# Kernel optimization log

Measured on AMD Instinct MI355X. Metric: run time of the kernel, lower is better.

## Reference

```python
import jax, jax.numpy as jnp
import numpy as np

N_NODES = 50000
N_EDGES = 600000
IN_DIM = 128
HID = 256
OUT = 3


def setup_inputs() -> dict:
    key = jax.random.key(0)
    ks = jax.random.split(key, 10)
    x = jax.random.normal(ks[0], (N_NODES, IN_DIM), dtype=jnp.float32)
    edge_index = jax.random.randint(ks[1], (2, N_EDGES), 0, N_NODES, dtype=jnp.int64)
    s = lambda k, shp: jax.random.normal(k, shp, dtype=jnp.float32) * (1.0 / np.sqrt(shp[0]))
    return {
        "x": x,
        "edge_index": edge_index,
        # SAGEConv1: lin_l (applied to aggregated neighbors, with bias), lin_r (root, no bias)
        "W1l": s(ks[2], (IN_DIM, HID)), "b1": jnp.zeros((HID,), jnp.float32), "W1r": s(ks[3], (IN_DIM, HID)),
        # SAGEConv2
        "W2l": s(ks[4], (HID, HID)), "b2": jnp.zeros((HID,), jnp.float32), "W2r": s(ks[5], (HID, HID)),
        # classification head
        "Wh": s(ks[6], (HID, OUT)), "bh": jnp.zeros((OUT,), jnp.float32),
    }


def _sage_conv(x, edge_index, Wl, b, Wr):
    """PyG SAGEConv with mean aggregation: out = lin_l(mean_{j->i} x_j) + lin_r(x_i)."""
    src, dst = edge_index[0], edge_index[1]
    n = x.shape[0]
    # gather source features and scatter-mean onto targets
    msg_sum = jax.ops.segment_sum(x[src], dst, num_segments=n)          # [N, d]
    deg = jax.ops.segment_sum(jnp.ones((src.shape[0],), x.dtype), dst, num_segments=n)
    mean = msg_sum / jnp.maximum(deg, 1.0)[:, None]                      # isolated nodes -> 0
    return mean @ Wl + b + x @ Wr


def reference(x, edge_index, W1l, b1, W1r, W2l, b2, W2r, Wh, bh):
    h = jax.nn.relu(_sage_conv(x, edge_index, W1l, b1, W1r))
    # dropout(p=0.2) is identity in eval mode
    h = jax.nn.relu(_sage_conv(h, edge_index, W2l, b2, W2r))
    return h @ Wh + bh
```

## Files before the change

### kernel.cpp

```cpp
#include <hip/hip_runtime.h>
#include <hip/hip_bf16.h>

#define N_NODES 50000
#define N_EDGES 600000
#define IN_DIM 128
#define HID 256
#define OUT_DIM 3

#define M_PAD 50048

#define SCAN_B 256
#define SCAN_NB ((N_NODES + SCAN_B - 1) / SCAN_B)

typedef __bf16 bf16x8 __attribute__((ext_vector_type(8)));
typedef float f32x4 __attribute__((ext_vector_type(4)));

static __device__ __forceinline__ unsigned short f2b(float f) {
    union { float f; unsigned u; } u; u.f = f;
    unsigned r = u.u + 0x7fffu + ((u.u >> 16) & 1u);
    return (unsigned short)(r >> 16);
}
static __device__ __forceinline__ float b2f(unsigned short b) {
    union { unsigned u; float f; } u; u.u = ((unsigned)b) << 16;
    return u.f;
}

static __device__ __forceinline__ size_t swz(int r, int k, int K) {
    return (((size_t)((r >> 4) * (K >> 5) + (k >> 5))) << 9)
         + ((((k >> 3) & 3) * 16 + (r & 15)) << 3) + (k & 7);
}


__global__ void count_deg_kernel(const int* __restrict__ dst, int* __restrict__ counts) {
    int e = blockIdx.x * blockDim.x + threadIdx.x;
    if (e < N_EDGES) atomicAdd(&counts[dst[e]], 1);
}

__global__ __launch_bounds__(256) void block_sum_kernel(const int* __restrict__ counts,
                                                        int* __restrict__ partial) {
    int node = blockIdx.x * SCAN_B + threadIdx.x;
    int v = (node < N_NODES) ? counts[node] : 0;
#pragma unroll
    for (int off = 32; off > 0; off >>= 1) v += __shfl_down(v, off);
    __shared__ int ws[4];
    if ((threadIdx.x & 63) == 0) ws[threadIdx.x >> 6] = v;
    __syncthreads();
    if (threadIdx.x == 0) partial[blockIdx.x] = ws[0] + ws[1] + ws[2] + ws[3];
}

__global__ __launch_bounds__(256) void scan_partial_kernel(int* __restrict__ partial) {
    __shared__ int s[SCAN_B];
    int t = threadIdx.x;
    int v = (t < SCAN_NB) ? partial[t] : 0;
    s[t] = v;
    __syncthreads();
    for (int off = 1; off < SCAN_B; off <<= 1) {
        int u = (t >= off) ? s[t - off] : 0;
        __syncthreads();
        s[t] += u;
        __syncthreads();
    }
    if (t < SCAN_NB) partial[t] = s[t] - v;
}

__global__ __launch_bounds__(256) void write_rowptr_kernel(const int* __restrict__ counts,
                                                           const int* __restrict__ partial,
                                                           int* __restrict__ row_ptr) {
    __shared__ int s[SCAN_B];
    int t = threadIdx.x;
    int node = blockIdx.x * SCAN_B + t;
    int v = (node < N_NODES) ? counts[node] : 0;
    s[t] = v;
    __syncthreads();
    for (int off = 1; off < SCAN_B; off <<= 1) {
        int u = (t >= off) ? s[t - off] : 0;
        __syncthreads();
        s[t] += u;
        __syncthreads();
    }
    if (node < N_NODES) row_ptr[node] = partial[blockIdx.x] + s[t] - v;
    if (node == 0) row_ptr[N_NODES] = N_EDGES;
}

__global__ void fill_csr_kernel(const int* __restrict__ src, const int* __restrict__ dst,
                                const int* __restrict__ row_ptr, int* __restrict__ cursor,
                                int* __restrict__ csr_src) {
    int e = blockIdx.x * blockDim.x + threadIdx.x;
    if (e < N_EDGES) {
        int d = dst[e];
        int pos = atomicAdd(&cursor[d], 1);
        csr_src[row_ptr[d] + pos] = src[e];
    }
}


__global__ void cast_f2b_kernel(const float* __restrict__ in,
                                unsigned short* __restrict__ out_row,
                                unsigned short* __restrict__ out_swz) {
    int i = blockIdx.x * blockDim.x + threadIdx.x;
    if (i * 4 < N_NODES * IN_DIM) {
        float4 v = ((const float4*)in)[i];
        ushort4 o;
        o.x = f2b(v.x); o.y = f2b(v.y); o.z = f2b(v.z); o.w = f2b(v.w);
        ((ushort4*)out_row)[i] = o;
        int m = i >> 5;
        int kb = (i & 31) * 4;
        *(ushort4*)(out_swz + swz(m, kb, IN_DIM)) = o;
    }
}

__global__ void tcast4_kernel(const float* __restrict__ W1l, const float* __restrict__ W1r,
                              const float* __restrict__ W2l, const float* __restrict__ W2r,
                              unsigned short* __restrict__ W1lt, unsigned short* __restrict__ W1rt,
                              unsigned short* __restrict__ W2lt, unsigned short* __restrict__ W2rt) {
    int i = blockIdx.x * blockDim.x + threadIdx.x;
    const float* in; unsigned short* out; int K, base;
    if (i < 32768)        { in = W1l; out = W1lt; K = IN_DIM; base = 0; }
    else if (i < 65536)   { in = W1r; out = W1rt; K = IN_DIM; base = 32768; }
    else if (i < 131072)  { in = W2l; out = W2lt; K = HID;    base = 65536; }
    else if (i < 196608)  { in = W2r; out = W2rt; K = HID;    base = 131072; }
    else return;
    int j = i - base;
    int k = j >> 8;
    int n = j & 255;
    out[swz(n, k, K)] = f2b(in[j]);
}

__global__ void init_out_kernel(const float* __restrict__ bh, float* __restrict__ out) {
    int i = blockIdx.x * blockDim.x + threadIdx.x;
    if (i < N_NODES * 3) out[i] = bh[i % 3];
}


static __device__ __forceinline__ void addv(float* acc, uint4 v) {
    acc[0] += b2f((unsigned short)(v.x & 0xffff));
    acc[1] += b2f((unsigned short)(v.x >> 16));
    acc[2] += b2f((unsigned short)(v.y & 0xffff));
    acc[3] += b2f((unsigned short)(v.y >> 16));
    acc[4] += b2f((unsigned short)(v.z & 0xffff));
    acc[5] += b2f((unsigned short)(v.z >> 16));
    acc[6] += b2f((unsigned short)(v.w & 0xffff));
    acc[7] += b2f((unsigned short)(v.w >> 16));
}

static __device__ __forceinline__ uint4 pack8(const float* a) {
    uint4 pk;
    pk.x = (unsigned)f2b(a[0]) | ((unsigned)f2b(a[1]) << 16);
    pk.y = (unsigned)f2b(a[2]) | ((unsigned)f2b(a[3]) << 16);
    pk.z = (unsigned)f2b(a[4]) | ((unsigned)f2b(a[5]) << 16);
    pk.w = (unsigned)f2b(a[6]) | ((unsigned)f2b(a[7]) << 16);
    return pk;
}

__global__ __launch_bounds__(256) void agg_mean256_kernel(const unsigned short* __restrict__ feat,
                                                          const int* __restrict__ row_ptr,
                                                          const int* __restrict__ csr_src,
                                                          unsigned short* __restrict__ out_swz) {
    int node = blockIdx.x * 4 + (threadIdx.x >> 6);
    if (node >= N_NODES) return;
    int lane = threadIdx.x & 63;
    int half = lane >> 5, lh = lane & 31;
    const uint4* f4 = (const uint4*)feat;
    float acc[8];
#pragma unroll
    for (int j = 0; j < 8; j++) acc[j] = 0.f;
    int beg = row_ptr[node], end = row_ptr[node + 1];
    int i = beg;
    for (; i + 4 <= end; i += 4) {
        int sA = csr_src[i + half];
        int sB = csr_src[i + 2 + half];
        uint4 vA = f4[(size_t)sA * 32 + lh];
        uint4 vB = f4[(size_t)sB * 32 + lh];
        addv(acc, vA);
        addv(acc, vB);
    }
    if (i + 2 <= end) {
        int s = csr_src[i + half];
        addv(acc, f4[(size_t)s * 32 + lh]);
        i += 2;
    }
    if (i < end && half == 0) {
        int s = csr_src[i];
        addv(acc, f4[(size_t)s * 32 + lh]);
    }
    float inv = (end > beg) ? 1.0f / (float)(end - beg) : 0.0f;
#pragma unroll
    for (int j = 0; j < 8; j++) {
        acc[j] += __shfl_xor(acc[j], 32);
        acc[j] *= inv;
    }
    if (half == 0) *(uint4*)(out_swz + swz(node, lh * 8, HID)) = pack8(acc);
}

__global__ __launch_bounds__(256) void agg_mean128_kernel(const unsigned short* __restrict__ feat,
                                                          const int* __restrict__ row_ptr,
                                                          const int* __restrict__ csr_src,
                                                          unsigned short* __restrict__ out_swz) {
    int node = blockIdx.x * 4 + (threadIdx.x >> 6);
    if (node >= N_NODES) return;
    int lane = threadIdx.x & 63;
    int q = lane >> 4, lq = lane & 15;
    const uint4* f4 = (const uint4*)feat;
    float acc[8];
#pragma unroll
    for (int j = 0; j < 8; j++) acc[j] = 0.f;
    int beg = row_ptr[node], end = row_ptr[node + 1];
    int i = beg;
    for (; i + 8 <= end; i += 8) {
        int sA = csr_src[i + q];
        int sB = csr_src[i + 4 + q];
        uint4 vA = f4[(size_t)sA * 16 + lq];
        uint4 vB = f4[(size_t)sB * 16 + lq];
        addv(acc, vA);
        addv(acc, vB);
    }
    if (i + 4 <= end) {
        int s = csr_src[i + q];
        addv(acc, f4[(size_t)s * 16 + lq]);
        i += 4;
    }
    int rem = end - i;
    if (q < rem) {
        int s = csr_src[i + q];
        addv(acc, f4[(size_t)s * 16 + lq]);
    }
    float inv = (end > beg) ? 1.0f / (float)(end - beg) : 0.0f;
#pragma unroll
    for (int j = 0; j < 8; j++) {
        acc[j] += __shfl_xor(acc[j], 32);
        acc[j] += __shfl_xor(acc[j], 16);
        acc[j] *= inv;
    }
    if (q == 0) *(uint4*)(out_swz + swz(node, lq * 8, IN_DIM)) = pack8(acc);
}


template <int KP>
static __device__ __forceinline__ void gemm_swz_core64(
    const unsigned short* __restrict__ A0, const unsigned short* __restrict__ B0,
    const unsigned short* __restrict__ A1, const unsigned short* __restrict__ B1,
    int tmw, int tn0, int l, f32x4 (&acc)[2][4]) {
    constexpr int KT = KP / 32;
    constexpr int TT = 2 * KT;
    bf16x8 a[2][2], b[2][4];

#define LDTILE(t_, s_)                                                                     \
    {                                                                                      \
        const unsigned short* A_ = ((t_) < KT) ? A0 : A1;                                  \
        const unsigned short* B_ = ((t_) < KT) ? B0 : B1;                                  \
        const int tk_ = ((t_) < KT) ? (t_) : (t_) - KT;                                    \
        a[s_][0] = *(const bf16x8*)(A_ + ((((size_t)tmw) * KT + tk_) << 9) + l * 8);       \
        a[s_][1] = *(const bf16x8*)(A_ + ((((size_t)(tmw + 1)) * KT + tk_) << 9) + l * 8); \
        _Pragma("unroll")                                                                  \
        for (int nt = 0; nt < 4; nt++)                                                     \
            b[s_][nt] = *(const bf16x8*)(B_ + ((((size_t)(tn0 + nt)) * KT + tk_) << 9) + l * 8); \
    }

    LDTILE(0, 0)
#pragma unroll
    for (int t = 0; t < TT; t++) {
        const int cur = t & 1;
        if (t + 1 < TT) LDTILE(t + 1, cur ^ 1)
#pragma unroll
        for (int mt = 0; mt < 2; mt++)
#pragma unroll
            for (int nt = 0; nt < 4; nt++)
                acc[mt][nt] = __builtin_amdgcn_mfma_f32_16x16x32_bf16(a[cur][mt], b[cur][nt],
                                                                      acc[mt][nt], 0, 0, 0);
    }
#undef LDTILE
}

template <int KP>
__global__ __launch_bounds__(256) void gemm_swz_kernel(
    const unsigned short* __restrict__ A0, const unsigned short* __restrict__ B0,
    const unsigned short* __restrict__ A1, const unsigned short* __restrict__ B1,
    const float* __restrict__ bias, unsigned short* __restrict__ out_row,
    unsigned short* __restrict__ out_swz, int M) {
    const int t = threadIdx.x;
    const int w = t >> 6, l = t & 63;
    const int quad = l >> 4, lr = l & 15;
    const int n0 = blockIdx.x * 64, m0 = blockIdx.y * 128;
    const int tmw = (m0 >> 4) + w * 2, tn0 = n0 >> 4;

    f32x4 acc[2][4];
    const f32x4 zero = {0.f, 0.f, 0.f, 0.f};
#pragma unroll
    for (int mt = 0; mt < 2; mt++)
#pragma unroll
        for (int nt = 0; nt < 4; nt++) acc[mt][nt] = zero;

    float bias_r[4];
#pragma unroll
    for (int nt = 0; nt < 4; nt++) bias_r[nt] = bias[n0 + nt * 16 + lr];

    gemm_swz_core64<KP>(A0, B0, A1, B1, tmw, tn0, l, acc);

#pragma unroll
    for (int mt = 0; mt < 2; mt++)
#pragma unroll
        for (int r = 0; r < 4; r++) {
            int gm = m0 + w * 32 + mt * 16 + quad * 4 + r;
            if (gm >= M) continue;
            unsigned short* orow = out_row + (size_t)gm * HID;
#pragma unroll
            for (int nt = 0; nt < 4; nt++) {
                int gn = n0 + nt * 16 + lr;
                unsigned short h = f2b(fmaxf(acc[mt][nt][r] + bias_r[nt], 0.f));
                orow[gn] = h;
                out_swz[swz(gm, gn, HID)] = h;
            }
        }
}

template <int KP>
__global__ __launch_bounds__(256) void gemm_swz_head_kernel(
    const unsigned short* __restrict__ A0, const unsigned short* __restrict__ B0,
    const unsigned short* __restrict__ A1, const unsigned short* __restrict__ B1,
    const float* __restrict__ bias, const float* __restrict__ Wh,
    float* __restrict__ out, int M) {
    const int t = threadIdx.x;
    const int w = t >> 6, l = t & 63;
    const int quad = l >> 4, lr = l & 15;
    const int n0 = blockIdx.x * 64, m0 = blockIdx.y * 128;
    const int tmw = (m0 >> 4) + w * 2, tn0 = n0 >> 4;

    f32x4 acc[2][4];
    const f32x4 zero = {0.f, 0.f, 0.f, 0.f};
#pragma unroll
    for (int mt = 0; mt < 2; mt++)
#pragma unroll
        for (int nt = 0; nt < 4; nt++) acc[mt][nt] = zero;

    float bias_r[4];
    float wh_r[4][3];
#pragma unroll
    for (int nt = 0; nt < 4; nt++) {
        int gn = n0 + nt * 16 + lr;
        bias_r[nt] = bias[gn];
        wh_r[nt][0] = Wh[gn * 3 + 0];
        wh_r[nt][1] = Wh[gn * 3 + 1];
        wh_r[nt][2] = Wh[gn * 3 + 2];
    }

    gemm_swz_core64<KP>(A0, B0, A1, B1, tmw, tn0, l, acc);

#pragma unroll
    for (int mt = 0; mt < 2; mt++)
#pragma unroll
        for (int r = 0; r < 4; r++) {
            int gm = m0 + w * 32 + mt * 16 + quad * 4 + r;
            float p0 = 0.f, p1 = 0.f, p2 = 0.f;
#pragma unroll
            for (int nt = 0; nt < 4; nt++) {
                float v = fmaxf(acc[mt][nt][r] + bias_r[nt], 0.f);
                p0 += v * wh_r[nt][0];
                p1 += v * wh_r[nt][1];
                p2 += v * wh_r[nt][2];
            }
#pragma unroll
            for (int off = 1; off < 16; off <<= 1) {
                p0 += __shfl_xor(p0, off);
                p1 += __shfl_xor(p1, off);
                p2 += __shfl_xor(p2, off);
            }
            if (lr == 0 && gm < M) {
                atomicAdd(&out[(size_t)gm * 3 + 0], p0);
                atomicAdd(&out[(size_t)gm * 3 + 1], p1);
                atomicAdd(&out[(size_t)gm * 3 + 2], p2);
            }
        }
}


extern "C" void kernel_launch(void* const* d_in, const int* in_sizes, int n_in,
                              void* d_out, int out_size, void* d_ws, size_t ws_size,
                              hipStream_t stream) {
    const float* x   = (const float*)d_in[0];
    const int*   ei  = (const int*)d_in[1];
    const int*   src = ei;
    const int*   dst = ei + N_EDGES;
    const float* W1l = (const float*)d_in[2];
    const float* b1  = (const float*)d_in[3];
    const float* W1r = (const float*)d_in[4];
    const float* W2l = (const float*)d_in[5];
    const float* b2  = (const float*)d_in[6];
    const float* W2r = (const float*)d_in[7];
    const float* Wh  = (const float*)d_in[8];
    const float* bh  = (const float*)d_in[9];
    float* out = (float*)d_out;

    char* ws = (char*)d_ws;
    size_t off = 0;
    auto alloc = [&](size_t bytes) -> void* {
        void* p = ws + off;
        off = (off + bytes + 255) & ~(size_t)255;
        return p;
    };
    int* counts   = (int*)alloc((size_t)N_NODES * 4);
    int* row_ptr  = (int*)alloc((size_t)(N_NODES + 1) * 4);
    int* cursor   = (int*)alloc((size_t)N_NODES * 4);
    int* partial  = (int*)alloc((size_t)SCAN_NB * 4);
    int* csr_src  = (int*)alloc((size_t)N_EDGES * 4);
    unsigned short* xb_row  = (unsigned short*)alloc((size_t)M_PAD * IN_DIM * 2);
    unsigned short* xb_swz  = (unsigned short*)alloc((size_t)M_PAD * IN_DIM * 2);
    unsigned short* agg1    = (unsigned short*)alloc((size_t)M_PAD * IN_DIM * 2);
    unsigned short* h1_row  = (unsigned short*)alloc((size_t)M_PAD * HID * 2);
    unsigned short* h1_swz  = (unsigned short*)alloc((size_t)M_PAD * HID * 2);
    unsigned short* agg2    = (unsigned short*)alloc((size_t)M_PAD * HID * 2);
    unsigned short* W1lt = (unsigned short*)alloc((size_t)IN_DIM * HID * 2);
    unsigned short* W1rt = (unsigned short*)alloc((size_t)IN_DIM * HID * 2);
    unsigned short* W2lt = (unsigned short*)alloc((size_t)HID * HID * 2);
    unsigned short* W2rt = (unsigned short*)alloc((size_t)HID * HID * 2);

    hipMemsetAsync(counts, 0, (size_t)N_NODES * 4, stream);
    hipMemsetAsync(cursor, 0, (size_t)N_NODES * 4, stream);

    const int eblocks = (N_EDGES + 255) / 256;
    count_deg_kernel<<<eblocks, 256, 0, stream>>>(dst, counts);
    block_sum_kernel<<<SCAN_NB, SCAN_B, 0, stream>>>(counts, partial);
    scan_partial_kernel<<<1, SCAN_B, 0, stream>>>(partial);
    write_rowptr_kernel<<<SCAN_NB, SCAN_B, 0, stream>>>(counts, partial, row_ptr);
    fill_csr_kernel<<<eblocks, 256, 0, stream>>>(src, dst, row_ptr, cursor, csr_src);

    {
        int n = N_NODES * IN_DIM;
        cast_f2b_kernel<<<(n / 4 + 255) / 256, 256, 0, stream>>>(x, xb_row, xb_swz);
        tcast4_kernel<<<(196608 + 255) / 256, 256, 0, stream>>>(W1l, W1r, W2l, W2r,
                                                                W1lt, W1rt, W2lt, W2rt);
        init_out_kernel<<<(N_NODES * 3 + 255) / 256, 256, 0, stream>>>(bh, out);
    }

    const int nblocks4 = (N_NODES + 3) / 4;
    dim3 gg(4, M_PAD / 128);

    agg_mean128_kernel<<<nblocks4, 256, 0, stream>>>(xb_row, row_ptr, csr_src, agg1);
    gemm_swz_kernel<IN_DIM><<<gg, 256, 0, stream>>>(agg1, W1lt, xb_swz, W1rt, b1,
                                                    h1_row, h1_swz, N_NODES);

    agg_mean256_kernel<<<nblocks4, 256, 0, stream>>>(h1_row, row_ptr, csr_src, agg2);
    gemm_swz_head_kernel<HID><<<gg, 256, 0, stream>>>(agg2, W2lt, h1_swz, W2rt, b2, Wh,
                                                      out, N_NODES);
}
```

Baseline: 311.9 us.

## Deepen GEMM register prefetch to 4 stages and remap blocks into grouped panels

The GEMM core now keeps four register buffers and prefetches three k-tiles ahead instead of double-buffering, so global load latency is better hidden behind MFMA work. The 2D grid becomes a 1D grid that groups 8 row panels with all 4 column tiles, so blocks that share A panels run close together and hit in L2. Launch bounds request 3 blocks per CU. The extra buffers raise register pressure, which may cut occupancy or cause spills.

Result: faster. 302.1 us (-3.2%).

```diff
diff --git a/kernel.cpp b/kernel.cpp
--- a/kernel.cpp
+++ b/kernel.cpp
@@ -8,6 +8,7 @@
 #define OUT_DIM 3
 
 #define M_PAD 50048
+#define N_PANELS 391
 
 #define SCAN_B 256
 #define SCAN_NB ((N_NODES + SCAN_B - 1) / SCAN_B)
@@ -236,31 +237,31 @@
 
 
 template <int KP>
-static __device__ __forceinline__ void gemm_swz_core64(
+static __device__ __forceinline__ void gemm_swz_core_pd4(
     const unsigned short* __restrict__ A0, const unsigned short* __restrict__ B0,
     const unsigned short* __restrict__ A1, const unsigned short* __restrict__ B1,
     int tmw, int tn0, int l, f32x4 (&acc)[2][4]) {
     constexpr int KT = KP / 32;
     constexpr int TT = 2 * KT;
-    bf16x8 a[2][2], b[2][4];
-
-#define LDTILE(t_, s_)                                                                     \
-    {                                                                                      \
-        const unsigned short* A_ = ((t_) < KT) ? A0 : A1;                                  \
-        const unsigned short* B_ = ((t_) < KT) ? B0 : B1;                                  \
-        const int tk_ = ((t_) < KT) ? (t_) : (t_) - KT;                                    \
-        a[s_][0] = *(const bf16x8*)(A_ + ((((size_t)tmw) * KT + tk_) << 9) + l * 8);       \
-        a[s_][1] = *(const bf16x8*)(A_ + ((((size_t)(tmw + 1)) * KT + tk_) << 9) + l * 8); \
-        _Pragma("unroll")                                                                  \
-        for (int nt = 0; nt < 4; nt++)                                                     \
-            b[s_][nt] = *(const bf16x8*)(B_ + ((((size_t)(tn0 + nt)) * KT + tk_) << 9) + l * 8); \
-    }
-
-    LDTILE(0, 0)
+    bf16x8 a[4][2], b[4][4];
+
+    auto ldtile = [&](int t_, int s_) {
+        const unsigned short* A_ = (t_ < KT) ? A0 : A1;
+        const unsigned short* B_ = (t_ < KT) ? B0 : B1;
+        const int tk_ = (t_ < KT) ? t_ : t_ - KT;
+        a[s_][0] = *(const bf16x8*)(A_ + ((((size_t)tmw) * KT + tk_) << 9) + l * 8);
+        a[s_][1] = *(const bf16x8*)(A_ + ((((size_t)(tmw + 1)) * KT + tk_) << 9) + l * 8);
+#pragma unroll
+        for (int nt = 0; nt < 4; nt++)
+            b[s_][nt] = *(const bf16x8*)(B_ + ((((size_t)(tn0 + nt)) * KT + tk_) << 9) + l * 8);
+    };
+
+#pragma unroll
+    for (int p = 0; p < 3; p++) ldtile(p, p);
 #pragma unroll
     for (int t = 0; t < TT; t++) {
-        const int cur = t & 1;
-        if (t + 1 < TT) LDTILE(t + 1, cur ^ 1)
+        const int cur = t & 3;
+        if (t + 3 < TT) ldtile(t + 3, (t + 3) & 3);
 #pragma unroll
         for (int mt = 0; mt < 2; mt++)
 #pragma unroll
@@ -268,19 +269,21 @@
                 acc[mt][nt] = __builtin_amdgcn_mfma_f32_16x16x32_bf16(a[cur][mt], b[cur][nt],
                                                                       acc[mt][nt], 0, 0, 0);
     }
-#undef LDTILE
 }
 
 template <int KP>
-__global__ __launch_bounds__(256) void gemm_swz_kernel(
+__global__ __launch_bounds__(256, 3) void gemm_swz_kernel(
     const unsigned short* __restrict__ A0, const unsigned short* __restrict__ B0,
     const unsigned short* __restrict__ A1, const unsigned short* __restrict__ B1,
     const float* __restrict__ bias, unsigned short* __restrict__ out_row,
     unsigned short* __restrict__ out_swz, int M) {
+    const int bid = blockIdx.x;
+    const int panel = (bid >> 5) * 8 + (bid & 7);
+    if (panel >= N_PANELS) return;
     const int t = threadIdx.x;
     const int w = t >> 6, l = t & 63;
     const int quad = l >> 4, lr = l & 15;
-    const int n0 = blockIdx.x * 64, m0 = blockIdx.y * 128;
+    const int m0 = panel * 128, n0 = ((bid >> 3) & 3) * 64;
     const int tmw = (m0 >> 4) + w * 2, tn0 = n0 >> 4;
 
     f32x4 acc[2][4];
@@ -294,7 +297,7 @@
 #pragma unroll
     for (int nt = 0; nt < 4; nt++) bias_r[nt] = bias[n0 + nt * 16 + lr];
 
-    gemm_swz_core64<KP>(A0, B0, A1, B1, tmw, tn0, l, acc);
+    gemm_swz_core_pd4<KP>(A0, B0, A1, B1, tmw, tn0, l, acc);
 
 #pragma unroll
     for (int mt = 0; mt < 2; mt++)
@@ -314,15 +317,18 @@
 }
 
 template <int KP>
-__global__ __launch_bounds__(256) void gemm_swz_head_kernel(
+__global__ __launch_bounds__(256, 3) void gemm_swz_head_kernel(
     const unsigned short* __restrict__ A0, const unsigned short* __restrict__ B0,
     const unsigned short* __restrict__ A1, const unsigned short* __restrict__ B1,
     const float* __restrict__ bias, const float* __restrict__ Wh,
     float* __restrict__ out, int M) {
+    const int bid = blockIdx.x;
+    const int panel = (bid >> 5) * 8 + (bid & 7);
+    if (panel >= N_PANELS) return;
     const int t = threadIdx.x;
     const int w = t >> 6, l = t & 63;
     const int quad = l >> 4, lr = l & 15;
-    const int n0 = blockIdx.x * 64, m0 = blockIdx.y * 128;
+    const int m0 = panel * 128, n0 = ((bid >> 3) & 3) * 64;
     const int tmw = (m0 >> 4) + w * 2, tn0 = n0 >> 4;
 
     f32x4 acc[2][4];
@@ -343,7 +349,7 @@
         wh_r[nt][2] = Wh[gn * 3 + 2];
     }
 
-    gemm_swz_core64<KP>(A0, B0, A1, B1, tmw, tn0, l, acc);
+    gemm_swz_core_pd4<KP>(A0, B0, A1, B1, tmw, tn0, l, acc);
 
 #pragma unroll
     for (int mt = 0; mt < 2; mt++)
@@ -432,13 +438,13 @@
     }
 
     const int nblocks4 = (N_NODES + 3) / 4;
-    dim3 gg(4, M_PAD / 128);
+    const int gemm_blocks = ((N_PANELS + 7) / 8) * 32;
 
     agg_mean128_kernel<<<nblocks4, 256, 0, stream>>>(xb_row, row_ptr, csr_src, agg1);
-    gemm_swz_kernel<IN_DIM><<<gg, 256, 0, stream>>>(agg1, W1lt, xb_swz, W1rt, b1,
-                                                    h1_row, h1_swz, N_NODES);
+    gemm_swz_kernel<IN_DIM><<<gemm_blocks, 256, 0, stream>>>(agg1, W1lt, xb_swz, W1rt, b1,
+                                                             h1_row, h1_swz, N_NODES);
 
     agg_mean256_kernel<<<nblocks4, 256, 0, stream>>>(h1_row, row_ptr, csr_src, agg2);
-    gemm_swz_head_kernel<HID><<<gg, 256, 0, stream>>>(agg2, W2lt, h1_swz, W2rt, b2, Wh,
-                                                      out, N_NODES);
-}
+    gemm_swz_head_kernel<HID><<<gemm_blocks, 256, 0, stream>>>(agg2, W2lt, h1_swz, W2rt, b2, Wh,
+                                                               out, N_NODES);
+}
```
